# Kernel tuning notes

Hardware: AMD Instinct MI355X
Metric: run time of the kernel (lower is better)

## Reference

```python
import jax, jax.numpy as jnp
import numpy as np
from jax import lax

BN_EPS = 1e-5

def conv_bn_prelu(x, w, b, scale, bias, a):
    # Conv2d(k=3, pad=1, stride=1) in NCHW / OIHW layout
    y = lax.conv_general_dilated(x, w, window_strides=(1, 1), padding='SAME',
                                 dimension_numbers=('NCHW', 'OIHW', 'NCHW'))
    y = y + b[None, :, None, None]
    # BatchNorm2d, training-mode batch statistics over (B, H, W)
    mean = jnp.mean(y, axis=(0, 2, 3), keepdims=True)
    var = jnp.var(y, axis=(0, 2, 3), keepdims=True)
    y = (y - mean) * lax.rsqrt(var + BN_EPS)
    y = y * scale[None, :, None, None] + bias[None, :, None, None]
    # PReLU with single shared slope parameter
    return jnp.where(y >= 0, y, a * y)

def setup_inputs() -> dict:
    key = jax.random.key(0)
    ks = jax.random.split(key, 7)
    B, C, H, W = 4, 64, 64, 64
    x = jax.random.normal(ks[0], (B, C, H, W), dtype=jnp.float32)
    conv_w = jax.random.normal(ks[1], (C, C, 3, 3), dtype=jnp.float32) * 0.05
    conv_b = jax.random.normal(ks[2], (C,), dtype=jnp.float32) * 0.05
    bn_scale = jax.random.uniform(ks[3], (C,), dtype=jnp.float32, minval=0.5, maxval=1.5)
    bn_bias = jax.random.normal(ks[4], (C,), dtype=jnp.float32) * 0.05
    prelu_a = jnp.full((1,), 0.25, dtype=jnp.float32)
    gamma = jax.random.normal(ks[5], (1,), dtype=jnp.float32)
    return {'x': x, 'conv_w': conv_w, 'conv_b': conv_b, 'bn_scale': bn_scale,
            'bn_bias': bn_bias, 'prelu_a': prelu_a, 'gamma': gamma}

def reference(x, conv_w, conv_b, bn_scale, bn_bias, prelu_a, gamma):
    B, C, H, W = x.shape
    N = H * W
    feat = conv_bn_prelu(x, conv_w, conv_b, bn_scale, bn_bias, prelu_a)  # (B,C,H,W)
    f = feat.reshape(B, C, N)  # proj_query = f^T, proj_key = f, proj_value = f
    # energy[b,i,j] = sum_c f[b,c,i] * f[b,c,j]  -> (B, N, N)
    energy = jnp.einsum('bci,bcj->bij', f, f)
    # energy_new = rowmax - energy, softmax over last dim
    energy_new = jnp.max(energy, axis=-1, keepdims=True) - energy
    attn = jax.nn.softmax(energy_new, axis=-1)
    # out = bmm(proj_value, attention^T): out[b,c,i] = sum_j f[b,c,j] * attn[b,i,j]
    out = jnp.einsum('bcj,bij->bci', f, attn).reshape(B, C, H, W)
    return gamma * out + feat
```

## Files before the change

### kernel.cpp

```cpp
#include <hip/hip_runtime.h>

constexpr int kB = 4, kC = 64, kH = 64, kW = 64, kN = kH * kW;
constexpr float kEps = 1e-5f;
constexpr int SPLIT = 4;

typedef __attribute__((ext_vector_type(8))) short short8;
typedef __attribute__((ext_vector_type(4))) float f32x4;
typedef unsigned short u16;

__device__ inline unsigned pkbf(float a, float b) {
  unsigned ua = __float_as_uint(a), ub = __float_as_uint(b);
  ua += 0x7fff + ((ua >> 16) & 1);
  ub += 0x7fff + ((ub >> 16) & 1);
  return (ua >> 16) | (ub & 0xffff0000u);
}

__global__ __launch_bounds__(256) void prep_w_kernel(const float* __restrict__ w,
                                                     u16* __restrict__ wA) {
  int idx = blockIdx.x * 256 + threadIdx.x;
  if (idx < 64 * 576) {
    int oc = idx / 576, r = idx - oc * 576;
    int khw = r >> 6, ic = r & 63;
    float v = w[(oc * 64 + ic) * 9 + khw];
    unsigned u = __float_as_uint(v);
    u += 0x7fff + ((u >> 16) & 1);
    wA[idx] = (u16)(u >> 16);
  }
}

__global__ __launch_bounds__(256) void conv_kernel(const float* __restrict__ x,
                                                   const u16* __restrict__ wA,
                                                   const float* __restrict__ bias,
                                                   float* __restrict__ y) {
  const int tid = threadIdx.x;
  const int lane = tid & 63;
  const int wv = tid >> 6;
  const int bx = blockIdx.x;
  const int b = bx >> 7;
  const int h = (bx & 127) >> 1;
  const int w0 = (bx & 1) * 32;
  const int lw = lane & 15, lg = lane >> 4;

  __shared__ __align__(16) u16 xt[3 * 40 * 64];

#pragma unroll
  for (int rep = 0; rep < 4; ++rep) {
    int idx = rep * 256 + tid;
    if (idx < 960) {
      int kh = idx / 320;
      int t = idx - kh * 320;
      int gw = t >> 5, icp = t & 31;
      int wb = w0 - 4 + gw * 4;
      int hh = h + kh - 1;
      float4 va = {0.f, 0.f, 0.f, 0.f}, vb = {0.f, 0.f, 0.f, 0.f};
      if (hh >= 0 && hh < 64 && wb >= 0 && wb < 64) {
        va = *(const float4*)&x[((b * 64 + icp * 2) * 64 + hh) * 64 + wb];
        vb = *(const float4*)&x[((b * 64 + icp * 2 + 1) * 64 + hh) * 64 + wb];
      }
      float av[4] = {va.x, va.y, va.z, va.w};
      float bv[4] = {vb.x, vb.y, vb.z, vb.w};
#pragma unroll
      for (int j = 0; j < 4; ++j) {
        int wc = gw * 4 + j;
        *(unsigned*)&xt[(kh * 40 + wc) * 64 + (((icp >> 2) ^ (wc & 7)) * 8 + (icp & 3) * 2)] =
            pkbf(av[j], bv[j]);
      }
    }
  }
  __syncthreads();

  const int oc0 = wv * 16;
  short8 af[18];
#pragma unroll
  for (int kc = 0; kc < 18; ++kc)
    af[kc] = *(const short8*)&wA[(oc0 + lw) * 576 + kc * 32 + lg * 8];

  f32x4 acc[2];
  acc[0] = (f32x4){0.f, 0.f, 0.f, 0.f};
  acc[1] = (f32x4){0.f, 0.f, 0.f, 0.f};
#pragma unroll
  for (int kc = 0; kc < 18; ++kc) {
    const int khw = kc >> 1;
    const int kh = khw / 3, kwv = khw % 3;
#pragma unroll
    for (int nt = 0; nt < 2; ++nt) {
      int wc = nt * 16 + lw + kwv + 3;
      short8 bf = *(const short8*)&xt[(kh * 40 + wc) * 64 + ((((kc & 1) * 4 + lg) ^ (wc & 7)) * 8)];
      acc[nt] = __builtin_amdgcn_mfma_f32_16x16x32_bf16(af[kc], bf, acc[nt], 0, 0, 0);
    }
  }
#pragma unroll
  for (int nt = 0; nt < 2; ++nt)
#pragma unroll
    for (int r = 0; r < 4; ++r) {
      int oc = oc0 + lg * 4 + r;
      y[((b * 64 + oc) * 64 + h) * 64 + w0 + nt * 16 + lw] = acc[nt][r] + bias[oc];
    }
}

__global__ __launch_bounds__(256) void stats_kernel(const float* __restrict__ y,
                                                    const float* __restrict__ scale,
                                                    const float* __restrict__ bias,
                                                    float* __restrict__ AB) {
  const int c = blockIdx.x;
  const int tid = threadIdx.x;
  float s = 0.f, s2 = 0.f;
  for (int b = 0; b < kB; ++b) {
    const float* p = y + (b * kC + c) * kN;
    for (int i = tid * 4; i < kN; i += 1024) {
      float4 v = *(const float4*)(p + i);
      s += v.x + v.y + v.z + v.w;
      s2 += v.x * v.x + v.y * v.y + v.z * v.z + v.w * v.w;
    }
  }
  __shared__ float rs[256], rq[256];
  rs[tid] = s;
  rq[tid] = s2;
  __syncthreads();
  for (int off = 128; off > 0; off >>= 1) {
    if (tid < off) { rs[tid] += rs[tid + off]; rq[tid] += rq[tid + off]; }
    __syncthreads();
  }
  if (tid == 0) {
    const float inv_n = 1.f / (float)(kB * kN);
    float mean = rs[0] * inv_n;
    float var = rq[0] * inv_n - mean * mean;
    float A = scale[c] * rsqrtf(var + kEps);
    AB[c] = A;
    AB[kC + c] = bias[c] - mean * A;
  }
}

__global__ __launch_bounds__(256) void pack_kernel(const float* __restrict__ y,
                                                   const float* __restrict__ AB,
                                                   const float* __restrict__ pa,
                                                   float* __restrict__ feat,
                                                   u16* __restrict__ fbfA,
                                                   u16* __restrict__ fbfB) {
  __shared__ float ls[64 * 65];
  const int tid = threadIdx.x;
  const int b = blockIdx.x >> 6;
  const int n0 = (blockIdx.x & 63) << 6;
  {
    const int c = tid >> 2, nj = (tid & 3) << 4;
    const float A = AB[c], Bc = AB[kC + c], a = pa[0];
    const float* yp = y + ((b * kC + c) * kN) + n0 + nj;
    float f[16];
#pragma unroll
    for (int v = 0; v < 4; ++v) {
      float4 xv = *(const float4*)(yp + v * 4);
      float t;
      t = fmaf(A, xv.x, Bc); f[v * 4 + 0] = t >= 0.f ? t : a * t;
      t = fmaf(A, xv.y, Bc); f[v * 4 + 1] = t >= 0.f ? t : a * t;
      t = fmaf(A, xv.z, Bc); f[v * 4 + 2] = t >= 0.f ? t : a * t;
      t = fmaf(A, xv.w, Bc); f[v * 4 + 3] = t >= 0.f ? t : a * t;
    }
    float* fo = feat + ((b * kC + c) * kN) + n0 + nj;
#pragma unroll
    for (int v = 0; v < 4; ++v) {
      float4 fv = {f[v * 4 + 0], f[v * 4 + 1], f[v * 4 + 2], f[v * 4 + 3]};
      *(float4*)(fo + v * 4) = fv;
    }
#pragma unroll
    for (int v = 0; v < 16; ++v) ls[c * 65 + nj + v] = f[v];
  }
  __syncthreads();
  {
    int chunk = tid >> 5, pt = chunk >> 1, kc = chunk & 1;
    int lp2 = (tid & 31) * 2;
    u16* dst = fbfA + ((size_t)((b * 256 + (n0 >> 4) + pt) * 2 + kc)) * 512;
#pragma unroll
    for (int e = 0; e < 2; ++e) {
      int L = lp2 + e;
      int n = pt * 16 + (L & 15);
      int cb = kc * 32 + (L >> 4) * 8;
      float v[8];
#pragma unroll
      for (int r = 0; r < 8; ++r) v[r] = ls[(cb + r) * 65 + n];
      uint4 o = {pkbf(v[0], v[1]), pkbf(v[2], v[3]), pkbf(v[4], v[5]), pkbf(v[6], v[7])};
      *(uint4*)&dst[L * 8] = o;
    }
  }
  {
    int chunk = tid >> 5, jt = chunk >> 2, ct = chunk & 3;
    int lp2 = (tid & 31) * 2;
    u16* dst = fbfB + ((size_t)((b * 128 + (n0 >> 5) + jt) * 4 + ct)) * 512;
#pragma unroll
    for (int e = 0; e < 2; ++e) {
      int L = lp2 + e;
      int c = ct * 16 + (L & 15);
      int nb = jt * 32 + (L >> 4) * 8;
      float v[8];
#pragma unroll
      for (int r = 0; r < 8; ++r) v[r] = ls[c * 65 + nb + r];
      uint4 o = {pkbf(v[0], v[1]), pkbf(v[2], v[3]), pkbf(v[4], v[5]), pkbf(v[6], v[7])};
      *(uint4*)&dst[L * 8] = o;
    }
  }
}

__global__ __launch_bounds__(256, 2) void attn_kernel(const u16* __restrict__ fbfA,
                                                      const u16* __restrict__ fbfB,
                                                      float* __restrict__ Op,
                                                      float* __restrict__ lp) {
  const int tid = threadIdx.x;
  const int lane = tid & 63;
  const int w = tid >> 6;
  const int bx = blockIdx.x;
  const int s = bx & 3, itb = (bx >> 2) & 15, b = bx >> 6;
  const int c15 = lane & 15, g = lane >> 4;

  __shared__ __align__(16) u16 Ps[4][64 * 40];
  u16* ps = &Ps[w][0];
  const int pw_off = c15 * 40 + g * 4;
  const int pr_off = c15 * 40 + g * 8;

  const uint4* fA = (const uint4*)fbfA;
  const uint4* fB = (const uint4*)fbfB;

  uint4 qf[4][2];
  const int ptq = itb * 16 + w * 4;
#pragma unroll
  for (int it = 0; it < 4; ++it)
#pragma unroll
    for (int kc = 0; kc < 2; ++kc) {
      uint4 q = fA[(size_t)((b * 256 + ptq + it) * 2 + kc) * 64 + lane];
      q.x ^= 0x80008000u; q.y ^= 0x80008000u; q.z ^= 0x80008000u; q.w ^= 0x80008000u;
      qf[it][kc] = q;
    }

  const short8 ones = {0x3F80, 0x3F80, 0x3F80, 0x3F80, 0x3F80, 0x3F80, 0x3F80, 0x3F80};

  f32x4 oacc[4][4];
  f32x4 lacc[4];
#pragma unroll
  for (int it = 0; it < 4; ++it) {
    lacc[it] = (f32x4){0.f, 0.f, 0.f, 0.f};
#pragma unroll
    for (int ct = 0; ct < 4; ++ct) oacc[it][ct] = (f32x4){0.f, 0.f, 0.f, 0.f};
  }

#pragma unroll 2
  for (int jj = 0; jj < 32; ++jj) {
    const int j0 = (s * 32 + jj) * 32;
    const int ca = (b * 256 + (j0 >> 4)) * 2;
    uint4 a00 = fA[(size_t)(ca + 0) * 64 + lane];
    uint4 a01 = fA[(size_t)(ca + 1) * 64 + lane];
    uint4 a10 = fA[(size_t)(ca + 2) * 64 + lane];
    uint4 a11 = fA[(size_t)(ca + 3) * 64 + lane];
    const int cb = (b * 128 + (j0 >> 5)) * 4;
    uint4 v0 = fB[(size_t)(cb + 0) * 64 + lane];
    uint4 v1 = fB[(size_t)(cb + 1) * 64 + lane];
    uint4 v2 = fB[(size_t)(cb + 2) * 64 + lane];
    uint4 v3 = fB[(size_t)(cb + 3) * 64 + lane];

    f32x4 sv[2][4];
#pragma unroll
    for (int it = 0; it < 4; ++it) {
      f32x4 z0 = (f32x4){0.f, 0.f, 0.f, 0.f};
      z0 = __builtin_amdgcn_mfma_f32_16x16x32_bf16(*(short8*)&a00, *(short8*)&qf[it][0], z0, 0, 0, 0);
      z0 = __builtin_amdgcn_mfma_f32_16x16x32_bf16(*(short8*)&a01, *(short8*)&qf[it][1], z0, 0, 0, 0);
      sv[0][it] = z0;
      f32x4 z1 = (f32x4){0.f, 0.f, 0.f, 0.f};
      z1 = __builtin_amdgcn_mfma_f32_16x16x32_bf16(*(short8*)&a10, *(short8*)&qf[it][0], z1, 0, 0, 0);
      z1 = __builtin_amdgcn_mfma_f32_16x16x32_bf16(*(short8*)&a11, *(short8*)&qf[it][1], z1, 0, 0, 0);
      sv[1][it] = z1;
    }
#pragma unroll
    for (int it = 0; it < 4; ++it)
#pragma unroll
      for (int jt = 0; jt < 2; ++jt) {
        float p0 = __expf(sv[jt][it][0]);
        float p1 = __expf(sv[jt][it][1]);
        float p2 = __expf(sv[jt][it][2]);
        float p3 = __expf(sv[jt][it][3]);
        uint2 d;
        d.x = __builtin_amdgcn_perm(__float_as_uint(p1), __float_as_uint(p0), 0x07060302u);
        d.y = __builtin_amdgcn_perm(__float_as_uint(p3), __float_as_uint(p2), 0x07060302u);
        *(uint2*)&ps[pw_off + it * 640 + jt * 16] = d;
      }
#pragma unroll
    for (int it = 0; it < 4; ++it) {
      short8 pf = *(const short8*)&ps[pr_off + it * 640];
      lacc[it] = __builtin_amdgcn_mfma_f32_16x16x32_bf16(pf, ones, lacc[it], 0, 0, 0);
      oacc[it][0] = __builtin_amdgcn_mfma_f32_16x16x32_bf16(pf, *(short8*)&v0, oacc[it][0], 0, 0, 0);
      oacc[it][1] = __builtin_amdgcn_mfma_f32_16x16x32_bf16(pf, *(short8*)&v1, oacc[it][1], 0, 0, 0);
      oacc[it][2] = __builtin_amdgcn_mfma_f32_16x16x32_bf16(pf, *(short8*)&v2, oacc[it][2], 0, 0, 0);
      oacc[it][3] = __builtin_amdgcn_mfma_f32_16x16x32_bf16(pf, *(short8*)&v3, oacc[it][3], 0, 0, 0);
    }
  }

  float* Ow = Op + (size_t)(bx * 4 + w) * 4096;
#pragma unroll
  for (int it = 0; it < 4; ++it)
#pragma unroll
    for (int ct = 0; ct < 4; ++ct)
#pragma unroll
      for (int r = 0; r < 4; ++r)
        Ow[(it * 16 + g * 4 + r) * 64 + ct * 16 + c15] = oacc[it][ct][r];
  if (c15 == 0) {
    float* lw_ = lp + (size_t)(bx * 4 + w) * 64;
#pragma unroll
    for (int it = 0; it < 4; ++it)
#pragma unroll
      for (int r = 0; r < 4; ++r) lw_[it * 16 + g * 4 + r] = lacc[it][r];
  }
}

__global__ __launch_bounds__(256) void combine_kernel(const float* __restrict__ Op,
                                                      const float* __restrict__ lp,
                                                      const float* __restrict__ feat,
                                                      const float* __restrict__ gamma_p,
                                                      float* __restrict__ out) {
  const int tid = threadIdx.x;
  const int bx = blockIdx.x;
  const int b = bx >> 6, it64 = bx & 63;
  const int itb = it64 >> 2, w = it64 & 3;
  const int gbase = (b * 16 + itb) * 16 + w;
  __shared__ float tr[64 * 65];
  __shared__ float linv[64];
  if (tid < 64) {
    float sum = 0.f;
    for (int s = 0; s < SPLIT; ++s) sum += lp[(size_t)(gbase + s * 4) * 64 + tid];
    linv[tid] = 1.f / sum;
  }
  __syncthreads();
  const float gm = gamma_p[0];
#pragma unroll
  for (int rr = 0; rr < 4; ++rr) {
    int flat4 = rr * 256 + tid;
    int i = flat4 >> 4, c4 = (flat4 & 15) * 4;
    float4 acc = {0.f, 0.f, 0.f, 0.f};
    for (int s = 0; s < SPLIT; ++s) {
      float4 v = *(const float4*)&Op[(size_t)(gbase + s * 4) * 4096 + i * 64 + c4];
      acc.x += v.x; acc.y += v.y; acc.z += v.z; acc.w += v.w;
    }
    float sc = gm * linv[i];
    tr[(c4 + 0) * 65 + i] = acc.x * sc;
    tr[(c4 + 1) * 65 + i] = acc.y * sc;
    tr[(c4 + 2) * 65 + i] = acc.z * sc;
    tr[(c4 + 3) * 65 + i] = acc.w * sc;
  }
  __syncthreads();
#pragma unroll
  for (int rr = 0; rr < 4; ++rr) {
    int flat4 = rr * 256 + tid;
    int c = flat4 >> 4, i4 = (flat4 & 15) * 4;
    float4 fv = *(const float4*)&feat[(size_t)(b * 64 + c) * 4096 + it64 * 64 + i4];
    float4 ov;
    ov.x = tr[c * 65 + i4 + 0] + fv.x;
    ov.y = tr[c * 65 + i4 + 1] + fv.y;
    ov.z = tr[c * 65 + i4 + 2] + fv.z;
    ov.w = tr[c * 65 + i4 + 3] + fv.w;
    *(float4*)&out[(size_t)(b * 64 + c) * 4096 + it64 * 64 + i4] = ov;
  }
}

extern "C" void kernel_launch(void* const* d_in, const int* in_sizes, int n_in,
                              void* d_out, int out_size, void* d_ws, size_t ws_size,
                              hipStream_t stream) {
  (void)in_sizes; (void)n_in; (void)out_size; (void)ws_size;
  const float* x        = (const float*)d_in[0];
  const float* conv_w   = (const float*)d_in[1];
  const float* conv_b   = (const float*)d_in[2];
  const float* bn_scale = (const float*)d_in[3];
  const float* bn_bias  = (const float*)d_in[4];
  const float* prelu_a  = (const float*)d_in[5];
  const float* gamma    = (const float*)d_in[6];
  float* out = (float*)d_out;

  float* feat = (float*)d_ws;
  u16* fbfA = (u16*)(feat + kB * kC * kN);
  u16* fbfB = fbfA + kB * kC * kN;
  float* AB = (float*)(fbfB + kB * kC * kN);
  u16* wA = (u16*)(AB + 256);
  float* Op = (float*)(wA + 36864);
  float* lp = Op + (size_t)256 * 4 * 4096;

  float* y = out;

  prep_w_kernel<<<144, 256, 0, stream>>>(conv_w, wA);
  conv_kernel<<<kB * kH * 2, 256, 0, stream>>>(x, wA, conv_b, y);
  stats_kernel<<<kC, 256, 0, stream>>>(y, bn_scale, bn_bias, AB);
  pack_kernel<<<kB * (kN / 64), 256, 0, stream>>>(y, AB, prelu_a, feat, fbfA, fbfB);
  attn_kernel<<<kB * 16 * SPLIT, 256, 0, stream>>>(fbfA, fbfB, Op, lp);
  combine_kernel<<<kB * 64, 256, 0, stream>>>(Op, lp, feat, gamma, out);
}
```

Baseline: 124.1 us.

## Fuse BN stats into conv, pre-scale queries for exp2, double split, pipeline attn loop

BatchNorm sums are now accumulated in the conv epilogue through shuffle reductions and binned atomics. This removes the separate stats kernel and its extra read of y. The pack kernel writes an extra bf16 copy of the features pre-scaled by -log2(e), so the attention kernel can use raw exp2 without the sign flip. The split over keys goes from 4 to 8 to put more blocks in flight, at the cost of a larger partial-output buffer and more combine traffic. The attention loop is software-pipelined so that each step's PV MFMAs overlap the next step's score MFMAs and loads.

```diff
diff --git a/kernel.cpp b/kernel.cpp
--- a/kernel.cpp
+++ b/kernel.cpp
@@ -2,7 +2,7 @@
 
 constexpr int kB = 4, kC = 64, kH = 64, kW = 64, kN = kH * kW;
 constexpr float kEps = 1e-5f;
-constexpr int SPLIT = 4;
+constexpr int SPLIT = 8;
 
 typedef __attribute__((ext_vector_type(8))) short short8;
 typedef __attribute__((ext_vector_type(4))) float f32x4;
@@ -14,6 +14,8 @@
   ub += 0x7fff + ((ub >> 16) & 1);
   return (ua >> 16) | (ub & 0xffff0000u);
 }
+
+__device__ inline float fexp2(float x) { return __builtin_amdgcn_exp2f(x); }
 
 __global__ __launch_bounds__(256) void prep_w_kernel(const float* __restrict__ w,
                                                      u16* __restrict__ wA) {
@@ -31,7 +33,8 @@
 __global__ __launch_bounds__(256) void conv_kernel(const float* __restrict__ x,
                                                    const u16* __restrict__ wA,
                                                    const float* __restrict__ bias,
-                                                   float* __restrict__ y) {
+                                                   float* __restrict__ y,
+                                                   float* __restrict__ sums) {
   const int tid = threadIdx.x;
   const int lane = tid & 63;
   const int wv = tid >> 6;
@@ -89,61 +92,73 @@
       acc[nt] = __builtin_amdgcn_mfma_f32_16x16x32_bf16(af[kc], bf, acc[nt], 0, 0, 0);
     }
   }
+  float yv[2][4];
+#pragma unroll
+  for (int r = 0; r < 4; ++r) {
+    float bv = bias[oc0 + lg * 4 + r];
+    yv[0][r] = acc[0][r] + bv;
+    yv[1][r] = acc[1][r] + bv;
+  }
 #pragma unroll
   for (int nt = 0; nt < 2; ++nt)
+#pragma unroll
+    for (int r = 0; r < 4; ++r)
+      y[((b * 64 + oc0 + lg * 4 + r) * 64 + h) * 64 + w0 + nt * 16 + lw] = yv[nt][r];
+  float sv[4], qv[4];
+#pragma unroll
+  for (int r = 0; r < 4; ++r) {
+    sv[r] = yv[0][r] + yv[1][r];
+    qv[r] = yv[0][r] * yv[0][r] + yv[1][r] * yv[1][r];
+  }
+#pragma unroll
+  for (int m = 1; m < 16; m <<= 1)
+#pragma unroll
+    for (int r = 0; r < 4; ++r) {
+      sv[r] += __shfl_xor(sv[r], m);
+      qv[r] += __shfl_xor(qv[r], m);
+    }
+  if (lw == 0) {
+    const int bin = bx & 7;
 #pragma unroll
     for (int r = 0; r < 4; ++r) {
       int oc = oc0 + lg * 4 + r;
-      y[((b * 64 + oc) * 64 + h) * 64 + w0 + nt * 16 + lw] = acc[nt][r] + bias[oc];
-    }
-}
-
-__global__ __launch_bounds__(256) void stats_kernel(const float* __restrict__ y,
-                                                    const float* __restrict__ scale,
-                                                    const float* __restrict__ bias,
-                                                    float* __restrict__ AB) {
-  const int c = blockIdx.x;
-  const int tid = threadIdx.x;
-  float s = 0.f, s2 = 0.f;
-  for (int b = 0; b < kB; ++b) {
-    const float* p = y + (b * kC + c) * kN;
-    for (int i = tid * 4; i < kN; i += 1024) {
-      float4 v = *(const float4*)(p + i);
-      s += v.x + v.y + v.z + v.w;
-      s2 += v.x * v.x + v.y * v.y + v.z * v.z + v.w * v.w;
-    }
-  }
-  __shared__ float rs[256], rq[256];
-  rs[tid] = s;
-  rq[tid] = s2;
-  __syncthreads();
-  for (int off = 128; off > 0; off >>= 1) {
-    if (tid < off) { rs[tid] += rs[tid + off]; rq[tid] += rq[tid + off]; }
-    __syncthreads();
-  }
-  if (tid == 0) {
-    const float inv_n = 1.f / (float)(kB * kN);
-    float mean = rs[0] * inv_n;
-    float var = rq[0] * inv_n - mean * mean;
-    float A = scale[c] * rsqrtf(var + kEps);
-    AB[c] = A;
-    AB[kC + c] = bias[c] - mean * A;
+      atomicAdd(&sums[bin * 128 + oc], sv[r]);
+      atomicAdd(&sums[bin * 128 + 64 + oc], qv[r]);
+    }
   }
 }
 
 __global__ __launch_bounds__(256) void pack_kernel(const float* __restrict__ y,
-                                                   const float* __restrict__ AB,
+                                                   const float* __restrict__ sums,
+                                                   const float* __restrict__ scale,
+                                                   const float* __restrict__ bias,
                                                    const float* __restrict__ pa,
                                                    float* __restrict__ feat,
                                                    u16* __restrict__ fbfA,
+                                                   u16* __restrict__ fbfQ,
                                                    u16* __restrict__ fbfB) {
   __shared__ float ls[64 * 65];
+  __shared__ float ABl[128];
   const int tid = threadIdx.x;
   const int b = blockIdx.x >> 6;
   const int n0 = (blockIdx.x & 63) << 6;
+  if (tid < 64) {
+    float s = 0.f, q = 0.f;
+#pragma unroll
+    for (int bin = 0; bin < 8; ++bin) {
+      s += sums[bin * 128 + tid];
+      q += sums[bin * 128 + 64 + tid];
+    }
+    float mean = s * (1.f / 16384.f);
+    float var = q * (1.f / 16384.f) - mean * mean;
+    float A = scale[tid] * rsqrtf(var + kEps);
+    ABl[tid] = A;
+    ABl[64 + tid] = bias[tid] - mean * A;
+  }
+  __syncthreads();
   {
     const int c = tid >> 2, nj = (tid & 3) << 4;
-    const float A = AB[c], Bc = AB[kC + c], a = pa[0];
+    const float A = ABl[c], Bc = ABl[64 + c], a = pa[0];
     const float* yp = y + ((b * kC + c) * kN) + n0 + nj;
     float f[16];
 #pragma unroll
@@ -168,7 +183,10 @@
   {
     int chunk = tid >> 5, pt = chunk >> 1, kc = chunk & 1;
     int lp2 = (tid & 31) * 2;
-    u16* dst = fbfA + ((size_t)((b * 256 + (n0 >> 4) + pt) * 2 + kc)) * 512;
+    size_t cidx = ((size_t)((b * 256 + (n0 >> 4) + pt) * 2 + kc)) * 512;
+    u16* dstA = fbfA + cidx;
+    u16* dstQ = fbfQ + cidx;
+    const float cl = -1.4426950408889634f;
 #pragma unroll
     for (int e = 0; e < 2; ++e) {
       int L = lp2 + e;
@@ -178,7 +196,10 @@
 #pragma unroll
       for (int r = 0; r < 8; ++r) v[r] = ls[(cb + r) * 65 + n];
       uint4 o = {pkbf(v[0], v[1]), pkbf(v[2], v[3]), pkbf(v[4], v[5]), pkbf(v[6], v[7])};
-      *(uint4*)&dst[L * 8] = o;
+      *(uint4*)&dstA[L * 8] = o;
+      uint4 oq = {pkbf(v[0] * cl, v[1] * cl), pkbf(v[2] * cl, v[3] * cl),
+                  pkbf(v[4] * cl, v[5] * cl), pkbf(v[6] * cl, v[7] * cl)};
+      *(uint4*)&dstQ[L * 8] = oq;
     }
   }
   {
@@ -200,6 +221,7 @@
 }
 
 __global__ __launch_bounds__(256, 2) void attn_kernel(const u16* __restrict__ fbfA,
+                                                      const u16* __restrict__ fbfQ,
                                                       const u16* __restrict__ fbfB,
                                                       float* __restrict__ Op,
                                                       float* __restrict__ lp) {
@@ -207,7 +229,7 @@
   const int lane = tid & 63;
   const int w = tid >> 6;
   const int bx = blockIdx.x;
-  const int s = bx & 3, itb = (bx >> 2) & 15, b = bx >> 6;
+  const int s = bx & 7, itb = (bx >> 3) & 15, b = bx >> 7;
   const int c15 = lane & 15, g = lane >> 4;
 
   __shared__ __align__(16) u16 Ps[4][64 * 40];
@@ -215,19 +237,17 @@
   const int pw_off = c15 * 40 + g * 4;
   const int pr_off = c15 * 40 + g * 8;
 
-  const uint4* fA = (const uint4*)fbfA;
-  const uint4* fB = (const uint4*)fbfB;
+  const uint4* fAb = (const uint4*)fbfA + (size_t)b * 32768 + lane;
+  const uint4* fQb = (const uint4*)fbfQ + (size_t)b * 32768 + lane;
+  const uint4* fBb = (const uint4*)fbfB + (size_t)b * 32768 + lane;
 
   uint4 qf[4][2];
   const int ptq = itb * 16 + w * 4;
 #pragma unroll
   for (int it = 0; it < 4; ++it)
 #pragma unroll
-    for (int kc = 0; kc < 2; ++kc) {
-      uint4 q = fA[(size_t)((b * 256 + ptq + it) * 2 + kc) * 64 + lane];
-      q.x ^= 0x80008000u; q.y ^= 0x80008000u; q.z ^= 0x80008000u; q.w ^= 0x80008000u;
-      qf[it][kc] = q;
-    }
+    for (int kc = 0; kc < 2; ++kc)
+      qf[it][kc] = fQb[(size_t)((ptq + it) * 2 + kc) * 64];
 
   const short8 ones = {0x3F80, 0x3F80, 0x3F80, 0x3F80, 0x3F80, 0x3F80, 0x3F80, 0x3F80};
 
@@ -240,20 +260,14 @@
     for (int ct = 0; ct < 4; ++ct) oacc[it][ct] = (f32x4){0.f, 0.f, 0.f, 0.f};
   }
 
-#pragma unroll 2
-  for (int jj = 0; jj < 32; ++jj) {
-    const int j0 = (s * 32 + jj) * 32;
-    const int ca = (b * 256 + (j0 >> 4)) * 2;
-    uint4 a00 = fA[(size_t)(ca + 0) * 64 + lane];
-    uint4 a01 = fA[(size_t)(ca + 1) * 64 + lane];
-    uint4 a10 = fA[(size_t)(ca + 2) * 64 + lane];
-    uint4 a11 = fA[(size_t)(ca + 3) * 64 + lane];
-    const int cb = (b * 128 + (j0 >> 5)) * 4;
-    uint4 v0 = fB[(size_t)(cb + 0) * 64 + lane];
-    uint4 v1 = fB[(size_t)(cb + 1) * 64 + lane];
-    uint4 v2 = fB[(size_t)(cb + 2) * 64 + lane];
-    uint4 v3 = fB[(size_t)(cb + 3) * 64 + lane];
-
+  const uint4* pA = fAb + (size_t)(s * 64) * 64;
+  const uint4* pV = fBb + (size_t)(s * 64) * 64;
+
+  uint4 vp0, vp1, vp2, vp3;
+  {
+    uint4 a00 = pA[0], a01 = pA[64], a10 = pA[128], a11 = pA[192];
+    vp0 = pV[0]; vp1 = pV[64]; vp2 = pV[128]; vp3 = pV[192];
+    pA += 256; pV += 256;
     f32x4 sv[2][4];
 #pragma unroll
     for (int it = 0; it < 4; ++it) {
@@ -269,24 +283,72 @@
 #pragma unroll
     for (int it = 0; it < 4; ++it)
 #pragma unroll
-      for (int jt = 0; jt < 2; ++jt) {
-        float p0 = __expf(sv[jt][it][0]);
-        float p1 = __expf(sv[jt][it][1]);
-        float p2 = __expf(sv[jt][it][2]);
-        float p3 = __expf(sv[jt][it][3]);
+      for (int jt2 = 0; jt2 < 2; ++jt2) {
+        float p0 = fexp2(sv[jt2][it][0]);
+        float p1 = fexp2(sv[jt2][it][1]);
+        float p2 = fexp2(sv[jt2][it][2]);
+        float p3 = fexp2(sv[jt2][it][3]);
         uint2 d;
         d.x = __builtin_amdgcn_perm(__float_as_uint(p1), __float_as_uint(p0), 0x07060302u);
         d.y = __builtin_amdgcn_perm(__float_as_uint(p3), __float_as_uint(p2), 0x07060302u);
-        *(uint2*)&ps[pw_off + it * 640 + jt * 16] = d;
+        *(uint2*)&ps[pw_off + it * 640 + jt2 * 16] = d;
       }
+  }
+
+#pragma unroll 2
+  for (int jt = 1; jt < 16; ++jt) {
+    short8 pf[4];
+#pragma unroll
+    for (int it = 0; it < 4; ++it) pf[it] = *(const short8*)&ps[pr_off + it * 640];
+    uint4 a00 = pA[0], a01 = pA[64], a10 = pA[128], a11 = pA[192];
+    uint4 vc0 = pV[0], vc1 = pV[64], vc2 = pV[128], vc3 = pV[192];
+    pA += 256; pV += 256;
 #pragma unroll
     for (int it = 0; it < 4; ++it) {
-      short8 pf = *(const short8*)&ps[pr_off + it * 640];
-      lacc[it] = __builtin_amdgcn_mfma_f32_16x16x32_bf16(pf, ones, lacc[it], 0, 0, 0);
-      oacc[it][0] = __builtin_amdgcn_mfma_f32_16x16x32_bf16(pf, *(short8*)&v0, oacc[it][0], 0, 0, 0);
-      oacc[it][1] = __builtin_amdgcn_mfma_f32_16x16x32_bf16(pf, *(short8*)&v1, oacc[it][1], 0, 0, 0);
-      oacc[it][2] = __builtin_amdgcn_mfma_f32_16x16x32_bf16(pf, *(short8*)&v2, oacc[it][2], 0, 0, 0);
-      oacc[it][3] = __builtin_amdgcn_mfma_f32_16x16x32_bf16(pf, *(short8*)&v3, oacc[it][3], 0, 0, 0);
+      lacc[it] = __builtin_amdgcn_mfma_f32_16x16x32_bf16(pf[it], ones, lacc[it], 0, 0, 0);
+      oacc[it][0] = __builtin_amdgcn_mfma_f32_16x16x32_bf16(pf[it], *(short8*)&vp0, oacc[it][0], 0, 0, 0);
+      oacc[it][1] = __builtin_amdgcn_mfma_f32_16x16x32_bf16(pf[it], *(short8*)&vp1, oacc[it][1], 0, 0, 0);
+      oacc[it][2] = __builtin_amdgcn_mfma_f32_16x16x32_bf16(pf[it], *(short8*)&vp2, oacc[it][2], 0, 0, 0);
+      oacc[it][3] = __builtin_amdgcn_mfma_f32_16x16x32_bf16(pf[it], *(short8*)&vp3, oacc[it][3], 0, 0, 0);
+    }
+    f32x4 sv[2][4];
+#pragma unroll
+    for (int it = 0; it < 4; ++it) {
+      f32x4 z0 = (f32x4){0.f, 0.f, 0.f, 0.f};
+      z0 = __builtin_amdgcn_mfma_f32_16x16x32_bf16(*(short8*)&a00, *(short8*)&qf[it][0], z0, 0, 0, 0);
+      z0 = __builtin_amdgcn_mfma_f32_16x16x32_bf16(*(short8*)&a01, *(short8*)&qf[it][1], z0, 0, 0, 0);
+      sv[0][it] = z0;
+      f32x4 z1 = (f32x4){0.f, 0.f, 0.f, 0.f};
+      z1 = __builtin_amdgcn_mfma_f32_16x16x32_bf16(*(short8*)&a10, *(short8*)&qf[it][0], z1, 0, 0, 0);
+      z1 = __builtin_amdgcn_mfma_f32_16x16x32_bf16(*(short8*)&a11, *(short8*)&qf[it][1], z1, 0, 0, 0);
+      sv[1][it] = z1;
+    }
+#pragma unroll
+    for (int it = 0; it < 4; ++it)
+#pragma unroll
+      for (int jt2 = 0; jt2 < 2; ++jt2) {
+        float p0 = fexp2(sv[jt2][it][0]);
+        float p1 = fexp2(sv[jt2][it][1]);
+        float p2 = fexp2(sv[jt2][it][2]);
+        float p3 = fexp2(sv[jt2][it][3]);
+        uint2 d;
+        d.x = __builtin_amdgcn_perm(__float_as_uint(p1), __float_as_uint(p0), 0x07060302u);
+        d.y = __builtin_amdgcn_perm(__float_as_uint(p3), __float_as_uint(p2), 0x07060302u);
+        *(uint2*)&ps[pw_off + it * 640 + jt2 * 16] = d;
+      }
+    vp0 = vc0; vp1 = vc1; vp2 = vc2; vp3 = vc3;
+  }
+  {
+    short8 pf[4];
+#pragma unroll
+    for (int it = 0; it < 4; ++it) pf[it] = *(const short8*)&ps[pr_off + it * 640];
+#pragma unroll
+    for (int it = 0; it < 4; ++it) {
+      lacc[it] = __builtin_amdgcn_mfma_f32_16x16x32_bf16(pf[it], ones, lacc[it], 0, 0, 0);
+      oacc[it][0] = __builtin_amdgcn_mfma_f32_16x16x32_bf16(pf[it], *(short8*)&vp0, oacc[it][0], 0, 0, 0);
+      oacc[it][1] = __builtin_amdgcn_mfma_f32_16x16x32_bf16(pf[it], *(short8*)&vp1, oacc[it][1], 0, 0, 0);
+      oacc[it][2] = __builtin_amdgcn_mfma_f32_16x16x32_bf16(pf[it], *(short8*)&vp2, oacc[it][2], 0, 0, 0);
+      oacc[it][3] = __builtin_amdgcn_mfma_f32_16x16x32_bf16(pf[it], *(short8*)&vp3, oacc[it][3], 0, 0, 0);
     }
   }
 
@@ -316,12 +378,13 @@
   const int bx = blockIdx.x;
   const int b = bx >> 6, it64 = bx & 63;
   const int itb = it64 >> 2, w = it64 & 3;
-  const int gbase = (b * 16 + itb) * 16 + w;
   __shared__ float tr[64 * 65];
   __shared__ float linv[64];
   if (tid < 64) {
     float sum = 0.f;
-    for (int s = 0; s < SPLIT; ++s) sum += lp[(size_t)(gbase + s * 4) * 64 + tid];
+#pragma unroll
+    for (int s = 0; s < SPLIT; ++s)
+      sum += lp[(size_t)(((b * 16 + itb) * 8 + s) * 4 + w) * 64 + tid];
     linv[tid] = 1.f / sum;
   }
   __syncthreads();
@@ -331,8 +394,9 @@
     int flat4 = rr * 256 + tid;
     int i = flat4 >> 4, c4 = (flat4 & 15) * 4;
     float4 acc = {0.f, 0.f, 0.f, 0.f};
+#pragma unroll
     for (int s = 0; s < SPLIT; ++s) {
-      float4 v = *(const float4*)&Op[(size_t)(gbase + s * 4) * 4096 + i * 64 + c4];
+      float4 v = *(const float4*)&Op[(size_t)(((b * 16 + itb) * 8 + s) * 4 + w) * 4096 + i * 64 + c4];
       acc.x += v.x; acc.y += v.y; acc.z += v.z; acc.w += v.w;
     }
     float sc = gm * linv[i];
@@ -371,18 +435,20 @@
 
   float* feat = (float*)d_ws;
   u16* fbfA = (u16*)(feat + kB * kC * kN);
-  u16* fbfB = fbfA + kB * kC * kN;
-  float* AB = (float*)(fbfB + kB * kC * kN);
-  u16* wA = (u16*)(AB + 256);
-  float* Op = (float*)(wA + 36864);
-  float* lp = Op + (size_t)256 * 4 * 4096;
+  u16* fbfQ = fbfA + kB * kC * kN;
+  u16* fbfB = fbfQ + kB * kC * kN;
+  u16* wA = fbfB + kB * kC * kN;
+  float* sums = (float*)(wA + 36864);
+  float* Op = sums + 1024;
+  float* lp = Op + (size_t)2048 * 4096;
 
   float* y = out;
 
+  (void)hipMemsetAsync(sums, 0, 1024 * sizeof(float), stream);
   prep_w_kernel<<<144, 256, 0, stream>>>(conv_w, wA);
-  conv_kernel<<<kB * kH * 2, 256, 0, stream>>>(x, wA, conv_b, y);
-  stats_kernel<<<kC, 256, 0, stream>>>(y, bn_scale, bn_bias, AB);
-  pack_kernel<<<kB * (kN / 64), 256, 0, stream>>>(y, AB, prelu_a, feat, fbfA, fbfB);
-  attn_kernel<<<kB * 16 * SPLIT, 256, 0, stream>>>(fbfA, fbfB, Op, lp);
+  conv_kernel<<<kB * kH * 2, 256, 0, stream>>>(x, wA, conv_b, y, sums);
+  pack_kernel<<<kB * (kN / 64), 256, 0, stream>>>(y, sums, bn_scale, bn_bias, prelu_a,
+                                                  feat, fbfA, fbfQ, fbfB);
+  attn_kernel<<<kB * 16 * SPLIT, 256, 0, stream>>>(fbfA, fbfQ, fbfB, Op, lp);
   combine_kernel<<<kB * 64, 256, 0, stream>>>(Op, lp, feat, gamma, out);
 }
```

After: 124.5 us. Within noise of the previous version (+0.3%).
